# Kernel tuning notes

Measured on AMD Instinct MI355X. Metric: run time of the kernel, lower is better.

## Reference

```python
import jax, jax.numpy as jnp
import numpy as np

NUM_EMBEDDINGS = 8192
EMBEDDING_DIM = 32
L2_EPS = 1e-12  # matches torch F.normalize eps


def _l2_normalize(x, axis=-1):
    norm = jnp.linalg.norm(x, axis=axis, keepdims=True)
    return x / jnp.maximum(norm, L2_EPS)


def setup_inputs() -> dict:
    key = jax.random.key(0)
    k1, k2 = jax.random.split(key)
    inputs = jax.random.normal(k1, (32, 1024, EMBEDDING_DIM), dtype=jnp.float32)
    embeddings = jax.random.normal(k2, (NUM_EMBEDDINGS, EMBEDDING_DIM), dtype=jnp.float32)
    embeddings = _l2_normalize(embeddings, axis=1)  # buffer init: F.normalize(randn)
    return {"inputs": inputs, "embeddings": embeddings}


def reference(inputs, embeddings):
    input_shape = inputs.shape
    d = embeddings.shape[1]
    flat = inputs.reshape(-1, d)                      # [N, d]
    flat_n = _l2_normalize(flat, axis=1)              # F.normalize(flat, p=2, dim=1)
    # cosine similarity against codebook: [N, K]
    distances = jnp.einsum('nd,kd->nk', flat_n, embeddings)
    encoding_indices = jnp.argmax(distances, axis=1)  # [N]
    quantized = embeddings[encoding_indices].reshape(input_shape)
    # use_commitment=False branch: mse(quantized, inputs.detach())
    loss = jnp.mean((quantized - jax.lax.stop_gradient(inputs)) ** 2)
    # straight-through estimator
    quantized_st = inputs + jax.lax.stop_gradient(quantized - inputs)
    return quantized_st, loss, encoding_indices.reshape(input_shape[:-1])
```

## Files before the change

kernel.cpp:

```cpp
#include <hip/hip_runtime.h>

typedef short short8 __attribute__((ext_vector_type(8)));
typedef float f32x4 __attribute__((ext_vector_type(4)));

#define NROWS 32768
#define DIM 32
#define KCODES 8192
#define FLAG_CAP 4096
#define EPS_REL (1.0f/8192.0f)

#define WS_EHI  0
#define WS_ELO  (512*1024)
#define WS_NORM (1024*1024)
#define WS_IDX  (WS_NORM + 128*1024)
#define WS_LIST (WS_IDX + 128*1024)
#define WS_CNT  (WS_LIST + FLAG_CAP*4)
#define WS_PART (WS_CNT + 64)

__device__ __forceinline__ unsigned short bf16_rne(float v){
    unsigned int u = __float_as_uint(v);
    unsigned int r = (u + 0x7fffu + ((u >> 16) & 1u)) >> 16;
    return (unsigned short)r;
}
__device__ __forceinline__ float bf16_to_f(unsigned short h){
    return __uint_as_float(((unsigned int)h) << 16);
}
__device__ __forceinline__ float dot4(const float4& a, const float4& b){
    return fmaf(a.w, b.w, fmaf(a.z, b.z, fmaf(a.y, b.y, a.x * b.x)));
}

__global__ __launch_bounds__(256) void vq_prep(
    const float* __restrict__ inputs, const float* __restrict__ emb,
    unsigned short* __restrict__ ehi, unsigned short* __restrict__ elo,
    float* __restrict__ norms, int* __restrict__ cnt)
{
    int tid = blockIdx.x * 256 + threadIdx.x;
    if (tid == 0) *cnt = 0;
    if (tid < NROWS){
        const float4* xr = (const float4*)(inputs + (size_t)tid * DIM);
        float s = 0.f;
        #pragma unroll
        for (int i = 0; i < 8; i++){ float4 v = xr[i]; s += v.x*v.x + v.y*v.y + v.z*v.z + v.w*v.w; }
        norms[tid] = sqrtf(s);
    } else if (tid < NROWS + KCODES){
        int r = tid - NROWS;
        const float* er = emb + (size_t)r * DIM;
        short8* dh = (short8*)(ehi + (size_t)r * DIM);
        short8* dl = (short8*)(elo + (size_t)r * DIM);
        #pragma unroll
        for (int i = 0; i < 4; i++){
            short8 a, b;
            #pragma unroll
            for (int j = 0; j < 8; j++){
                float v = er[i*8 + j];
                unsigned short h = bf16_rne(v);
                a[j] = (short)h;
                b[j] = (short)bf16_rne(v - bf16_to_f(h));
            }
            dh[i] = a; dl[i] = b;
        }
    }
}

__global__ __launch_bounds__(512, 4) void vq_main_mfma(
    const float* __restrict__ inputs,
    const unsigned short* __restrict__ ehi,
    const unsigned short* __restrict__ elo,
    const float* __restrict__ norms,
    int* __restrict__ idxws, int* __restrict__ list, int* __restrict__ cnt)
{
    const int L = threadIdx.x & 63;
    const int w = threadIdx.x >> 6;
    const int rowbase = blockIdx.x * 64;

    short8 ahi[4], alo[4];
    #pragma unroll
    for (int rg = 0; rg < 4; ++rg){
        const float* xr = inputs + (size_t)(rowbase + rg*16 + (L & 15)) * DIM + (L >> 4) * 8;
        float4 p0 = *(const float4*)xr;
        float4 p1 = *(const float4*)(xr + 4);
        float f[8] = {p0.x, p0.y, p0.z, p0.w, p1.x, p1.y, p1.z, p1.w};
        short8 h, l;
        #pragma unroll
        for (int i = 0; i < 8; i++){
            unsigned short hb = bf16_rne(f[i]);
            h[i] = (short)hb;
            l[i] = (short)bf16_rne(f[i] - bf16_to_f(hb));
        }
        ahi[rg] = h; alo[rg] = l;
    }

    float v1[16], v2[16]; int i1[16];
    #pragma unroll
    for (int r = 0; r < 16; r++){ v1[r] = -3.0e38f; v2[r] = -3.0e38f; i1[r] = 0; }

    const int codebase = w * (KCODES / 8);
    const unsigned short* ehp = ehi + (size_t)(codebase + (L & 15)) * DIM + (L >> 4) * 8;
    const unsigned short* elp = elo + (size_t)(codebase + (L & 15)) * DIM + (L >> 4) * 8;

    for (int t = 0; t < 64; ++t){
        short8 bh = *(const short8*)(ehp + t * 16 * DIM);
        short8 bl = *(const short8*)(elp + t * 16 * DIM);
        int kv = codebase + t * 16 + (L & 15);
        #pragma unroll
        for (int rg = 0; rg < 4; ++rg){
            f32x4 acc = {0.f, 0.f, 0.f, 0.f};
            acc = __builtin_amdgcn_mfma_f32_16x16x32_bf16(ahi[rg], bh, acc, 0, 0, 0);
            acc = __builtin_amdgcn_mfma_f32_16x16x32_bf16(ahi[rg], bl, acc, 0, 0, 0);
            acc = __builtin_amdgcn_mfma_f32_16x16x32_bf16(alo[rg], bh, acc, 0, 0, 0);
            #pragma unroll
            for (int q = 0; q < 4; q++){
                int r = rg * 4 + q;
                float sc = acc[q];
                bool gt = sc > v1[r];
                v2[r] = __builtin_amdgcn_fmed3f(sc, v1[r], v2[r]);
                v1[r] = gt ? sc : v1[r];
                i1[r] = gt ? kv : i1[r];
            }
        }
    }

    #pragma unroll
    for (int m = 1; m < 16; m <<= 1){
        #pragma unroll
        for (int r = 0; r < 16; r++){
            float ov1 = __shfl_xor(v1[r], m, 64);
            int   oi1 = __shfl_xor(i1[r], m, 64);
            float ov2 = __shfl_xor(v2[r], m, 64);
            float mn = fminf(v1[r], ov1);
            v2[r] = fmaxf(fmaxf(v2[r], ov2), mn);
            bool g = ov1 > v1[r];
            v1[r] = g ? ov1 : v1[r];
            i1[r] = g ? oi1 : i1[r];
        }
    }

    __shared__ float sv1[8][64];
    __shared__ float sv2[8][64];
    __shared__ int   si1[8][64];
    if ((L & 15) == 0){
        #pragma unroll
        for (int rg = 0; rg < 4; rg++){
            #pragma unroll
            for (int q = 0; q < 4; q++){
                int rl = rg * 16 + (L >> 4) * 4 + q;
                sv1[w][rl] = v1[rg*4 + q];
                sv2[w][rl] = v2[rg*4 + q];
                si1[w][rl] = i1[rg*4 + q];
            }
        }
    }
    __syncthreads();

    if (threadIdx.x < 64){
        int rl = threadIdx.x;
        float bv1 = -3.0e38f, bv2 = -3.0e38f; int bi = 0;
        #pragma unroll
        for (int s = 0; s < 8; s++){
            float a1 = sv1[s][rl], a2 = sv2[s][rl]; int ai = si1[s][rl];
            float mn = fminf(bv1, a1);
            bv2 = fmaxf(fmaxf(bv2, a2), mn);
            bool g = a1 > bv1;
            bv1 = g ? a1 : bv1;
            bi  = g ? ai : bi;
        }
        int row = rowbase + rl;
        idxws[row] = bi;
        float eps = norms[row] * EPS_REL;
        if (bv1 - bv2 <= eps){
            int pos = atomicAdd(cnt, 1);
            if (pos < FLAG_CAP) list[pos] = row;
        }
    }
}

__global__ __launch_bounds__(256) void vq_refine(
    const float* __restrict__ inputs, const float* __restrict__ emb,
    int* __restrict__ idxws, const int* __restrict__ list, const int* __restrict__ cnt)
{
    int n = *cnt; if (n > FLAG_CAP) n = FLAG_CAP;
    __shared__ float sv[4]; __shared__ int si[4];
    for (int j = blockIdx.x; j < n; j += gridDim.x){
        int row = list[j];
        const float4* xr = (const float4*)(inputs + (size_t)row * DIM);
        float4 x0 = xr[0], x1 = xr[1], x2 = xr[2], x3 = xr[3];
        float4 x4 = xr[4], x5 = xr[5], x6 = xr[6], x7 = xr[7];
        float bv = -3.0e38f; int bi = 0x7fffffff;
        for (int c = threadIdx.x; c < KCODES; c += 256){
            const float4* ep = (const float4*)(emb + (size_t)c * DIM);
            float d = dot4(x0, ep[0]) + dot4(x1, ep[1]) + dot4(x2, ep[2]) + dot4(x3, ep[3])
                    + dot4(x4, ep[4]) + dot4(x5, ep[5]) + dot4(x6, ep[6]) + dot4(x7, ep[7]);
            if (d > bv || (d == bv && c < bi)){ bv = d; bi = c; }
        }
        #pragma unroll
        for (int off = 32; off; off >>= 1){
            float ov = __shfl_down(bv, off, 64);
            int   oi = __shfl_down(bi, off, 64);
            if (ov > bv || (ov == bv && oi < bi)){ bv = ov; bi = oi; }
        }
        if ((threadIdx.x & 63) == 0){ sv[threadIdx.x >> 6] = bv; si[threadIdx.x >> 6] = bi; }
        __syncthreads();
        if (threadIdx.x == 0){
            #pragma unroll
            for (int q = 1; q < 4; q++){
                if (sv[q] > bv || (sv[q] == bv && si[q] < bi)){ bv = sv[q]; bi = si[q]; }
            }
            idxws[row] = bi;
        }
        __syncthreads();
    }
}

__global__ __launch_bounds__(256) void vq_output(
    const float* __restrict__ inputs, const float* __restrict__ emb,
    const int* __restrict__ idxws,
    float* __restrict__ out_q, float* __restrict__ out_idx, float* __restrict__ part)
{
    int row = blockIdx.x * 256 + threadIdx.x;
    int idx = idxws[row];
    const float4* ep = (const float4*)(emb + (size_t)idx * DIM);
    const float4* xr = (const float4*)(inputs + (size_t)row * DIM);
    float4* oq = (float4*)(out_q + (size_t)row * DIM);
    float s = 0.f;
    #pragma unroll
    for (int i = 0; i < 8; i++){
        float4 q = ep[i], x = xr[i];
        oq[i] = q;
        float dx = q.x - x.x, dy = q.y - x.y, dz = q.z - x.z, dw = q.w - x.w;
        s += dx*dx + dy*dy + dz*dz + dw*dw;
    }
    out_idx[row] = (float)idx;
    #pragma unroll
    for (int off = 32; off; off >>= 1) s += __shfl_down(s, off, 64);
    __shared__ float sp[4];
    if ((threadIdx.x & 63) == 0) sp[threadIdx.x >> 6] = s;
    __syncthreads();
    if (threadIdx.x == 0) part[blockIdx.x] = sp[0] + sp[1] + sp[2] + sp[3];
}

__global__ void vq_loss(const float* __restrict__ part, float* __restrict__ out_loss){
    float s = 0.f;
    for (int i = threadIdx.x; i < 128; i += 64) s += part[i];
    #pragma unroll
    for (int off = 32; off; off >>= 1) s += __shfl_down(s, off, 64);
    if (threadIdx.x == 0) *out_loss = s * (1.0f / ((float)NROWS * (float)DIM));
}

extern "C" void kernel_launch(void* const* d_in, const int* in_sizes, int n_in,
                              void* d_out, int out_size, void* d_ws, size_t ws_size,
                              hipStream_t stream) {
    const float* inputs = (const float*)d_in[0];
    const float* emb    = (const float*)d_in[1];
    float* out      = (float*)d_out;
    float* out_q    = out;
    float* out_loss = out + (size_t)NROWS * DIM;
    float* out_idx  = out_loss + 1;

    char* ws = (char*)d_ws;
    unsigned short* ehi   = (unsigned short*)(ws + WS_EHI);
    unsigned short* elo   = (unsigned short*)(ws + WS_ELO);
    float*          norms = (float*)(ws + WS_NORM);
    int*            idxws = (int*)(ws + WS_IDX);
    int*            list  = (int*)(ws + WS_LIST);
    int*            cnt   = (int*)(ws + WS_CNT);
    float*          part  = (float*)(ws + WS_PART);

    vq_prep     <<<dim3((NROWS + KCODES + 255) / 256), dim3(256), 0, stream>>>(inputs, emb, ehi, elo, norms, cnt);
    vq_main_mfma<<<dim3(NROWS / 64),                   dim3(512), 0, stream>>>(inputs, ehi, elo, norms, idxws, list, cnt);
    vq_refine   <<<dim3(512),                          dim3(256), 0, stream>>>(inputs, emb, idxws, list, cnt);
    vq_output   <<<dim3(NROWS / 256),                  dim3(256), 0, stream>>>(inputs, emb, idxws, out_q, out_idx, part);
    vq_loss     <<<dim3(1),                            dim3(64),  0, stream>>>(part, out_loss);
}
```

Before: 109.6 us.

## Pack code index into score bits, fuse norms into main and loss into output

The per-row input norms are now computed inside the main MFMA kernel and shared through LDS, so the prep kernel only converts the codebook. The argmax tracks scores as unsigned integers with the tile index packed into the low 6 mantissa bits, after adding a 2*norm bias to keep them positive. This drops the separate index registers and selects. The cross-lane shuffle reduction is replaced by an LDS-based two-stage reduction, and the final loss kernel is folded into the output kernel with a last-block ticket. The near-tie tolerance is widened to absorb the truncated mantissa bits, which may send more rows to the refine pass.

Result: faster. 103.9 us (-5.1%).

```diff
diff --git a/kernel.cpp b/kernel.cpp
--- a/kernel.cpp
+++ b/kernel.cpp
@@ -7,12 +7,11 @@
 #define DIM 32
 #define KCODES 8192
 #define FLAG_CAP 4096
-#define EPS_REL (1.0f/8192.0f)
+#define EPS_REL (1.0f/4096.0f)
 
 #define WS_EHI  0
 #define WS_ELO  (512*1024)
-#define WS_NORM (1024*1024)
-#define WS_IDX  (WS_NORM + 128*1024)
+#define WS_IDX  (1024*1024)
 #define WS_LIST (WS_IDX + 128*1024)
 #define WS_CNT  (WS_LIST + FLAG_CAP*4)
 #define WS_PART (WS_CNT + 64)
@@ -30,48 +29,67 @@
 }
 
 __global__ __launch_bounds__(256) void vq_prep(
-    const float* __restrict__ inputs, const float* __restrict__ emb,
+    const float* __restrict__ emb,
     unsigned short* __restrict__ ehi, unsigned short* __restrict__ elo,
-    float* __restrict__ norms, int* __restrict__ cnt)
+    int* __restrict__ cnt)
 {
-    int tid = blockIdx.x * 256 + threadIdx.x;
-    if (tid == 0) *cnt = 0;
-    if (tid < NROWS){
-        const float4* xr = (const float4*)(inputs + (size_t)tid * DIM);
-        float s = 0.f;
-        #pragma unroll
-        for (int i = 0; i < 8; i++){ float4 v = xr[i]; s += v.x*v.x + v.y*v.y + v.z*v.z + v.w*v.w; }
-        norms[tid] = sqrtf(s);
-    } else if (tid < NROWS + KCODES){
-        int r = tid - NROWS;
-        const float* er = emb + (size_t)r * DIM;
-        short8* dh = (short8*)(ehi + (size_t)r * DIM);
-        short8* dl = (short8*)(elo + (size_t)r * DIM);
-        #pragma unroll
-        for (int i = 0; i < 4; i++){
-            short8 a, b;
-            #pragma unroll
-            for (int j = 0; j < 8; j++){
-                float v = er[i*8 + j];
-                unsigned short h = bf16_rne(v);
-                a[j] = (short)h;
-                b[j] = (short)bf16_rne(v - bf16_to_f(h));
-            }
-            dh[i] = a; dl[i] = b;
-        }
-    }
-}
+    int r = blockIdx.x * 256 + threadIdx.x;
+    if (r < 2) cnt[r] = 0;
+    const float* er = emb + (size_t)r * DIM;
+    short8* dh = (short8*)(ehi + (size_t)r * DIM);
+    short8* dl = (short8*)(elo + (size_t)r * DIM);
+    #pragma unroll
+    for (int i = 0; i < 4; i++){
+        float4 v0 = *(const float4*)(er + i*8);
+        float4 v1 = *(const float4*)(er + i*8 + 4);
+        float f[8] = {v0.x, v0.y, v0.z, v0.w, v1.x, v1.y, v1.z, v1.w};
+        short8 a, b;
+        #pragma unroll
+        for (int j = 0; j < 8; j++){
+            unsigned short h = bf16_rne(f[j]);
+            a[j] = (short)h;
+            b[j] = (short)bf16_rne(f[j] - bf16_to_f(h));
+        }
+        dh[i] = a; dl[i] = b;
+    }
+}
+
+#define PROC(bh, bl, tcs)                                                        \
+  {                                                                              \
+    unsigned int tcv = (unsigned int)(tcs);                                      \
+    _Pragma("unroll")                                                            \
+    for (int rg = 0; rg < 4; ++rg){                                              \
+      f32x4 acc = __builtin_amdgcn_mfma_f32_16x16x32_bf16(ahi[rg], bh, cbias[rg], 0, 0, 0); \
+      acc = __builtin_amdgcn_mfma_f32_16x16x32_bf16(ahi[rg], bl, acc, 0, 0, 0);  \
+      acc = __builtin_amdgcn_mfma_f32_16x16x32_bf16(alo[rg], bh, acc, 0, 0, 0);  \
+      _Pragma("unroll")                                                          \
+      for (int q = 0; q < 4; ++q){                                               \
+        unsigned int u = (__float_as_uint(acc[q]) & maskv) | tcv;                \
+        int rr = rg * 4 + q;                                                     \
+        unsigned int nv2;                                                        \
+        asm("v_med3_u32 %0, %1, %2, %3" : "=v"(nv2) : "v"(u), "v"(v1[rr]), "v"(v2[rr])); \
+        v2[rr] = nv2;                                                            \
+        v1[rr] = (u > v1[rr]) ? u : v1[rr];                                      \
+      }                                                                          \
+    }                                                                            \
+  }
 
 __global__ __launch_bounds__(512, 4) void vq_main_mfma(
     const float* __restrict__ inputs,
     const unsigned short* __restrict__ ehi,
     const unsigned short* __restrict__ elo,
-    const float* __restrict__ norms,
     int* __restrict__ idxws, int* __restrict__ list, int* __restrict__ cnt)
 {
     const int L = threadIdx.x & 63;
     const int w = threadIdx.x >> 6;
     const int rowbase = blockIdx.x * 64;
+
+    __shared__ float snorm[64];
+    __shared__ unsigned int sv1[8][64][17];
+    __shared__ unsigned int sv2[8][64][17];
+    __shared__ unsigned int pb1[8][64];
+    __shared__ unsigned int pb2[8][64];
+    __shared__ int          pbc[8][64];
 
     short8 ahi[4], alo[4];
     #pragma unroll
@@ -88,86 +106,93 @@
             l[i] = (short)bf16_rne(f[i] - bf16_to_f(hb));
         }
         ahi[rg] = h; alo[rg] = l;
-    }
-
-    float v1[16], v2[16]; int i1[16];
-    #pragma unroll
-    for (int r = 0; r < 16; r++){ v1[r] = -3.0e38f; v2[r] = -3.0e38f; i1[r] = 0; }
-
-    const int codebase = w * (KCODES / 8);
-    const unsigned short* ehp = ehi + (size_t)(codebase + (L & 15)) * DIM + (L >> 4) * 8;
-    const unsigned short* elp = elo + (size_t)(codebase + (L & 15)) * DIM + (L >> 4) * 8;
-
-    for (int t = 0; t < 64; ++t){
-        short8 bh = *(const short8*)(ehp + t * 16 * DIM);
-        short8 bl = *(const short8*)(elp + t * 16 * DIM);
-        int kv = codebase + t * 16 + (L & 15);
-        #pragma unroll
-        for (int rg = 0; rg < 4; ++rg){
-            f32x4 acc = {0.f, 0.f, 0.f, 0.f};
-            acc = __builtin_amdgcn_mfma_f32_16x16x32_bf16(ahi[rg], bh, acc, 0, 0, 0);
-            acc = __builtin_amdgcn_mfma_f32_16x16x32_bf16(ahi[rg], bl, acc, 0, 0, 0);
-            acc = __builtin_amdgcn_mfma_f32_16x16x32_bf16(alo[rg], bh, acc, 0, 0, 0);
-            #pragma unroll
-            for (int q = 0; q < 4; q++){
-                int r = rg * 4 + q;
-                float sc = acc[q];
-                bool gt = sc > v1[r];
-                v2[r] = __builtin_amdgcn_fmed3f(sc, v1[r], v2[r]);
-                v1[r] = gt ? sc : v1[r];
-                i1[r] = gt ? kv : i1[r];
-            }
-        }
-    }
-
-    #pragma unroll
-    for (int m = 1; m < 16; m <<= 1){
-        #pragma unroll
-        for (int r = 0; r < 16; r++){
-            float ov1 = __shfl_xor(v1[r], m, 64);
-            int   oi1 = __shfl_xor(i1[r], m, 64);
-            float ov2 = __shfl_xor(v2[r], m, 64);
-            float mn = fminf(v1[r], ov1);
-            v2[r] = fmaxf(fmaxf(v2[r], ov2), mn);
-            bool g = ov1 > v1[r];
-            v1[r] = g ? ov1 : v1[r];
-            i1[r] = g ? oi1 : i1[r];
-        }
-    }
-
-    __shared__ float sv1[8][64];
-    __shared__ float sv2[8][64];
-    __shared__ int   si1[8][64];
-    if ((L & 15) == 0){
-        #pragma unroll
-        for (int rg = 0; rg < 4; rg++){
-            #pragma unroll
-            for (int q = 0; q < 4; q++){
-                int rl = rg * 16 + (L >> 4) * 4 + q;
-                sv1[w][rl] = v1[rg*4 + q];
-                sv2[w][rl] = v2[rg*4 + q];
-                si1[w][rl] = i1[rg*4 + q];
-            }
-        }
+        float s = dot4(p0, p0) + dot4(p1, p1);
+        s += __shfl_xor(s, 16, 64);
+        s += __shfl_xor(s, 32, 64);
+        if (w == 0 && (L >> 4) == 0) snorm[rg*16 + L] = sqrtf(s);
+    }
+    __syncthreads();
+
+    f32x4 cbias[4];
+    #pragma unroll
+    for (int rg = 0; rg < 4; ++rg){
+        #pragma unroll
+        for (int q = 0; q < 4; ++q)
+            cbias[rg][q] = 2.0f * snorm[rg*16 + (L >> 4)*4 + q];
+    }
+
+    unsigned int maskv = 0xFFFFFFC0u;
+    asm("" : "+v"(maskv));
+
+    unsigned int v1[16], v2[16];
+    #pragma unroll
+    for (int r = 0; r < 16; r++){ v1[r] = 0u; v2[r] = 0u; }
+
+    const unsigned short* ehp = ehi + (size_t)(w*1024 + (L & 15)) * DIM + (L >> 4) * 8;
+    const unsigned short* elp = elo + (size_t)(w*1024 + (L & 15)) * DIM + (L >> 4) * 8;
+
+    for (int t = 0; t < 64; t += 2){
+        short8 bh0 = *(const short8*)(ehp);
+        short8 bl0 = *(const short8*)(elp);
+        short8 bh1 = *(const short8*)(ehp + 512);
+        short8 bl1 = *(const short8*)(elp + 512);
+        ehp += 1024; elp += 1024;
+        PROC(bh0, bl0, 63 - t);
+        PROC(bh1, bl1, 62 - t);
+    }
+
+    #pragma unroll
+    for (int rg = 0; rg < 4; ++rg){
+        #pragma unroll
+        for (int q = 0; q < 4; ++q){
+            int row = rg*16 + (L >> 4)*4 + q;
+            sv1[w][row][L & 15] = v1[rg*4 + q];
+            sv2[w][row][L & 15] = v2[rg*4 + q];
+        }
+    }
+    __syncthreads();
+
+    {
+        int r = threadIdx.x & 63;
+        int s = threadIdx.x >> 6;
+        unsigned int b1 = 0u, b2 = 0u; int bc = 0;
+        #pragma unroll
+        for (int c = 0; c < 16; ++c){
+            unsigned int u1 = sv1[s][r][c];
+            unsigned int u2 = sv2[s][r][c];
+            unsigned int mn = min(b1, u1);
+            unsigned int mx = max(b2, u2);
+            b2 = max(mn, mx);
+            bool g = u1 > b1;
+            b1 = g ? u1 : b1;
+            bc = g ? c : bc;
+        }
+        pb1[s][r] = b1; pb2[s][r] = b2; pbc[s][r] = bc;
     }
     __syncthreads();
 
     if (threadIdx.x < 64){
-        int rl = threadIdx.x;
-        float bv1 = -3.0e38f, bv2 = -3.0e38f; int bi = 0;
-        #pragma unroll
-        for (int s = 0; s < 8; s++){
-            float a1 = sv1[s][rl], a2 = sv2[s][rl]; int ai = si1[s][rl];
-            float mn = fminf(bv1, a1);
-            bv2 = fmaxf(fmaxf(bv2, a2), mn);
-            bool g = a1 > bv1;
-            bv1 = g ? a1 : bv1;
-            bi  = g ? ai : bi;
-        }
-        int row = rowbase + rl;
-        idxws[row] = bi;
-        float eps = norms[row] * EPS_REL;
-        if (bv1 - bv2 <= eps){
+        int r = threadIdx.x;
+        unsigned int b1 = 0u, b2 = 0u; int bw = 0, bc = 0;
+        #pragma unroll
+        for (int s = 0; s < 8; ++s){
+            unsigned int u1 = pb1[s][r];
+            unsigned int u2 = pb2[s][r];
+            unsigned int mn = min(b1, u1);
+            unsigned int mx = max(b2, u2);
+            b2 = max(mn, mx);
+            bool g = u1 > b1;
+            b1 = g ? u1 : b1;
+            bw = g ? s : bw;
+            bc = g ? pbc[s][r] : bc;
+        }
+        int t = 63 - (int)(b1 & 63u);
+        int k = bw*1024 + t*16 + bc;
+        int row = rowbase + r;
+        idxws[row] = k;
+        float f1 = __uint_as_float(b1 & 0xFFFFFFC0u);
+        float f2 = __uint_as_float(b2 & 0xFFFFFFC0u);
+        if (f1 - f2 <= snorm[r] * EPS_REL){
             int pos = atomicAdd(cnt, 1);
             if (pos < FLAG_CAP) list[pos] = row;
         }
@@ -214,7 +239,8 @@
 __global__ __launch_bounds__(256) void vq_output(
     const float* __restrict__ inputs, const float* __restrict__ emb,
     const int* __restrict__ idxws,
-    float* __restrict__ out_q, float* __restrict__ out_idx, float* __restrict__ part)
+    float* __restrict__ out_q, float* __restrict__ out_idx,
+    float* __restrict__ part, int* __restrict__ ticket, float* __restrict__ out_loss)
 {
     int row = blockIdx.x * 256 + threadIdx.x;
     int idx = idxws[row];
@@ -233,17 +259,23 @@
     #pragma unroll
     for (int off = 32; off; off >>= 1) s += __shfl_down(s, off, 64);
     __shared__ float sp[4];
+    __shared__ int tkt;
     if ((threadIdx.x & 63) == 0) sp[threadIdx.x >> 6] = s;
     __syncthreads();
-    if (threadIdx.x == 0) part[blockIdx.x] = sp[0] + sp[1] + sp[2] + sp[3];
-}
-
-__global__ void vq_loss(const float* __restrict__ part, float* __restrict__ out_loss){
-    float s = 0.f;
-    for (int i = threadIdx.x; i < 128; i += 64) s += part[i];
-    #pragma unroll
-    for (int off = 32; off; off >>= 1) s += __shfl_down(s, off, 64);
-    if (threadIdx.x == 0) *out_loss = s * (1.0f / ((float)NROWS * (float)DIM));
+    if (threadIdx.x == 0){
+        part[blockIdx.x] = sp[0] + sp[1] + sp[2] + sp[3];
+        __threadfence();
+        tkt = atomicAdd(ticket, 1);
+    }
+    __syncthreads();
+    if (tkt == (NROWS/256) - 1 && threadIdx.x < 64){
+        __threadfence();
+        float t = 0.f;
+        for (int i = threadIdx.x; i < NROWS/256; i += 64) t += part[i];
+        #pragma unroll
+        for (int off = 32; off; off >>= 1) t += __shfl_down(t, off, 64);
+        if (threadIdx.x == 0) *out_loss = t * (1.0f / ((float)NROWS * (float)DIM));
+    }
 }
 
 extern "C" void kernel_launch(void* const* d_in, const int* in_sizes, int n_in,
@@ -259,15 +291,13 @@
     char* ws = (char*)d_ws;
     unsigned short* ehi   = (unsigned short*)(ws + WS_EHI);
     unsigned short* elo   = (unsigned short*)(ws + WS_ELO);
-    float*          norms = (float*)(ws + WS_NORM);
     int*            idxws = (int*)(ws + WS_IDX);
     int*            list  = (int*)(ws + WS_LIST);
     int*            cnt   = (int*)(ws + WS_CNT);
     float*          part  = (float*)(ws + WS_PART);
 
-    vq_prep     <<<dim3((NROWS + KCODES + 255) / 256), dim3(256), 0, stream>>>(inputs, emb, ehi, elo, norms, cnt);
-    vq_main_mfma<<<dim3(NROWS / 64),                   dim3(512), 0, stream>>>(inputs, ehi, elo, norms, idxws, list, cnt);
-    vq_refine   <<<dim3(512),                          dim3(256), 0, stream>>>(inputs, emb, idxws, list, cnt);
-    vq_output   <<<dim3(NROWS / 256),                  dim3(256), 0, stream>>>(inputs, emb, idxws, out_q, out_idx, part);
-    vq_loss     <<<dim3(1),                            dim3(64),  0, stream>>>(part, out_loss);
-}
+    vq_prep     <<<dim3(KCODES/256), dim3(256), 0, stream>>>(emb, ehi, elo, cnt);
+    vq_main_mfma<<<dim3(NROWS/64),   dim3(512), 0, stream>>>(inputs, ehi, elo, idxws, list, cnt);
+    vq_refine   <<<dim3(256),        dim3(256), 0, stream>>>(inputs, emb, idxws, list, cnt);
+    vq_output   <<<dim3(NROWS/256),  dim3(256), 0, stream>>>(inputs, emb, idxws, out_q, out_idx, part, cnt + 1, out_loss);
+}
```
